# Performance work log

Hardware: AMD Instinct MI355X
Metric: run time of the kernel (lower is better)

## Reference

```python
import jax, jax.numpy as jnp
import numpy as np

BN_EPS = 1e-5


def setup_inputs() -> dict:
    key = jax.random.key(0)
    ks = jax.random.split(key, 8)
    B, C, H, W = 8, 512, 48, 48
    P = 64
    s_in = 1.0 / np.sqrt(C)
    s_p = 1.0 / np.sqrt(P)
    return {
        "x": jax.random.normal(ks[0], (B, C, H, W), dtype=jnp.float32),
        "Wq": jax.random.uniform(ks[1], (P, C), jnp.float32, -s_in, s_in),
        "Wk": jax.random.uniform(ks[2], (P, C), jnp.float32, -s_in, s_in),
        "Wv": jax.random.uniform(ks[3], (C, C), jnp.float32, -s_in, s_in),
        "align_w": jax.random.uniform(ks[4], (P,), jnp.float32, -s_p, s_p),
        "Wfc": jax.random.uniform(ks[5], (C, C), jnp.float32, -s_in, s_in),
        "bfc": jax.random.uniform(ks[6], (C,), jnp.float32, -s_in, s_in),
        "gamma": jnp.ones((C,), jnp.float32),
        "beta": jnp.zeros((C,), jnp.float32),
    }


def reference(x, Wq, Wk, Wv, align_w, Wfc, bfc, gamma, beta):
    B, C, H, W = x.shape
    N = H * W
    px = jnp.transpose(x.reshape(B, C, N), (0, 2, 1))  # [B, N, C]

    q = jnp.tanh(px @ Wq.T)  # [B, N, P]
    k = jnp.tanh(px @ Wk.T)  # [B, N, P]
    v = px @ Wv.T            # [B, N, C]

    # align(q_i * k_j) = sum_p q[b,i,p] * k[b,j,p] * align_w[p]
    scores = jnp.einsum('bip,bjp,p->bij', q, k, align_w)  # [B, N, N]
    attn = jax.nn.softmax(scores, axis=2)

    content = px + attn @ v           # [B, N, C]
    content = content @ Wfc.T + bfc   # fc
    c = jnp.transpose(content, (0, 2, 1)).reshape(B, C, H, W)

    # BatchNorm2d in training mode: batch statistics over (B, H, W), biased var
    mean = jnp.mean(c, axis=(0, 2, 3), keepdims=True)
    var = jnp.var(c, axis=(0, 2, 3), keepdims=True)
    g = gamma.reshape(1, C, 1, 1)
    b = beta.reshape(1, C, 1, 1)
    out = g * (c - mean) * jax.lax.rsqrt(var + BN_EPS) + b
    return jax.nn.relu(out)
```

## Files before the change

kernel.cpp:

```cpp
#include <hip/hip_runtime.h>
#include <stdint.h>

#define BB 8
#define CC 512
#define NN 2304
#define NT16 (NN / 16)
#define NT32 (NN / 32)
#define CT32 (CC / 32)
#define NYB 48

typedef float f32x4 __attribute__((ext_vector_type(4)));
typedef short s16x8 __attribute__((ext_vector_type(8)));

__device__ __forceinline__ unsigned short f2bf(float f) {
  union { float f; uint32_t u; } v; v.f = f;
  uint32_t u = v.u;
  return (unsigned short)((u + 0x7FFFu + ((u >> 16) & 1u)) >> 16);
}
__device__ __forceinline__ float bf2f(unsigned short b) {
  union { uint32_t u; float f; } v; v.u = ((uint32_t)b) << 16;
  return v.f;
}


__global__ void k_prep_w(const float* __restrict__ Wq, const float* __restrict__ Wk,
                         const float* __restrict__ Wv, const float* __restrict__ Wfc,
                         unsigned short* __restrict__ wcat_t, unsigned short* __restrict__ wfc_t) {
  int idx = blockIdx.x * 256 + threadIdx.x;
  const int tot_cat = 640 * 512;
  if (idx < tot_cat) {
    int tile = idx >> 9, inner = idx & 511;
    int j = (tile >> 4) * 16 + (inner >> 5);
    int k = (tile & 15) * 32 + (inner & 31);
    float v = (j < 64) ? Wq[j * 512 + k] : ((j < 128) ? Wk[(j - 64) * 512 + k] : Wv[(j - 128) * 512 + k]);
    wcat_t[idx] = f2bf(v);
  } else if (idx < tot_cat + 512 * 512) {
    int i2 = idx - tot_cat;
    int tile = i2 >> 9, inner = i2 & 511;
    int j = (tile >> 4) * 16 + (inner >> 5);
    int k = (tile & 15) * 32 + (inner & 31);
    wfc_t[i2] = f2bf(Wfc[j * 512 + k]);
  }
}

__global__ void k_px(const float* __restrict__ x, unsigned short* __restrict__ px_t) {
  __shared__ float t[32][33];
  int b = blockIdx.x;
  int nb = blockIdx.y * 32;
  int cb = blockIdx.z * 32;
  int lane = threadIdx.x & 31;
  int row = threadIdx.x >> 5;
  const float* xb = x + (size_t)b * CC * NN;
  for (int rr = 0; rr < 4; rr++) {
    int c = cb + row + 8 * rr;
    t[row + 8 * rr][lane] = xb[(size_t)c * NN + nb + lane];
  }
  __syncthreads();
  int rbase = (b * NN + nb) >> 4;
  int ct = cb >> 5;
  for (int rr = 0; rr < 4; rr++) {
    int nl = row + 8 * rr;
    size_t off = ((size_t)(rbase + (nl >> 4)) * CT32 + ct) * 512 + (nl & 15) * 32 + lane;
    px_t[off] = f2bf(t[lane][nl]);
  }
}

__global__ __launch_bounds__(256, 2) void k_qkv(const unsigned short* __restrict__ px_t,
                                                const unsigned short* __restrict__ wcat_t,
                                                const float* __restrict__ align_w,
                                                unsigned short* __restrict__ q_t,
                                                unsigned short* __restrict__ k_t,
                                                unsigned short* __restrict__ v_row) {
  int b = blockIdx.x;
  int nb = blockIdx.y * 64;
  int jb0 = blockIdx.z * 128;
  int tid = threadIdx.x;
  int w = tid >> 6, l = tid & 63, l15 = l & 15, lq = l >> 4;
  int jw = jb0 + 32 * w;
  int loff = l15 * 32 + 8 * lq;
  int rA = (b * NN + nb) >> 4;
  f32x4 acc[4][2];
  for (int mf = 0; mf < 4; mf++) for (int nf = 0; nf < 2; nf++) acc[mf][nf] = (f32x4){0.f, 0.f, 0.f, 0.f};
  for (int kk = 0; kk < 16; kk++) {
    s16x8 a[4], bbf[2];
    for (int mf = 0; mf < 4; mf++)
      a[mf] = *(const s16x8*)(px_t + ((size_t)(rA + mf) * CT32 + kk) * 512 + loff);
    for (int nf = 0; nf < 2; nf++)
      bbf[nf] = *(const s16x8*)(wcat_t + ((size_t)((jw >> 4) + nf) * CT32 + kk) * 512 + loff);
    for (int mf = 0; mf < 4; mf++)
      for (int nf = 0; nf < 2; nf++)
        acc[mf][nf] = __builtin_amdgcn_mfma_f32_16x16x32_bf16(a[mf], bbf[nf], acc[mf][nf], 0, 0, 0);
  }
  for (int mf = 0; mf < 4; mf++)
    for (int nf = 0; nf < 2; nf++)
      for (int r = 0; r < 4; r++) {
        int j = jw + 16 * nf + l15;
        int nl = 4 * lq + r;
        float v = acc[mf][nf][r];
        if (j < 128) { v = tanhf(v); if (j < 64) v *= align_w[j]; }
        unsigned short bv = f2bf(v);
        if (j < 64)
          q_t[((size_t)(rA + mf) * 2 + (j >> 5)) * 512 + nl * 32 + (j & 31)] = bv;
        else if (j < 128) {
          int jj = j - 64;
          k_t[((size_t)(rA + mf) * 2 + (jj >> 5)) * 512 + nl * 32 + (jj & 31)] = bv;
        } else {
          v_row[((size_t)(b * NN) + nb + 16 * mf + nl) * 512 + (j - 128)] = bv;
        }
      }
}

__global__ void k_vt(const unsigned short* __restrict__ v_row, unsigned short* __restrict__ vt_t) {
  __shared__ uint32_t t[32][33];
  int b = blockIdx.x;
  int nb = blockIdx.y * 32;
  int cb = blockIdx.z * 32;
  int lane = threadIdx.x & 31;
  int row = threadIdx.x >> 5;
  const unsigned short* src = v_row + (size_t)b * NN * 512;
  for (int rr = 0; rr < 4; rr++) {
    int n = nb + row + 8 * rr;
    t[row + 8 * rr][lane] = (uint32_t)src[(size_t)n * 512 + cb + lane];
  }
  __syncthreads();
  unsigned short* dst = vt_t + (size_t)b * (CC / 16) * NT32 * 512;
  for (int rr = 0; rr < 4; rr++) {
    int c = cb + row + 8 * rr;
    size_t off = ((size_t)(c >> 4) * NT32 + (nb >> 5)) * 512 + (c & 15) * 32 + lane;
    dst[off] = (unsigned short)t[lane][row + 8 * rr];
  }
}

__global__ __launch_bounds__(256, 3) void k_attn(const unsigned short* __restrict__ q_t,
                                                 const unsigned short* __restrict__ k_t,
                                                 const unsigned short* __restrict__ vt_t,
                                                 unsigned short* __restrict__ px_t ) {
  __shared__ __align__(16) unsigned short e_s[2][48 * 64];
  __shared__ float rs_s[4][48];
  int b = blockIdx.x;
  int ib = blockIdx.y * 48;
  int ch = blockIdx.z * 256;
  int tid = threadIdx.x;
  int w = tid >> 6, l = tid & 63, l15 = l & 15, lq = l >> 4;
  int c0 = ch + 64 * w;
  int loff = l15 * 32 + 8 * lq;
  int rQ = (b * NN + ib) >> 4;
  int ktb = b * NT16;
  const unsigned short* vb = vt_t + (size_t)b * (CC / 16) * NT32 * 512;

  s16x8 qa[3][2];
  for (int mf = 0; mf < 3; mf++)
    for (int ks = 0; ks < 2; ks++)
      qa[mf][ks] = *(const s16x8*)(q_t + ((size_t)(rQ + mf) * 2 + ks) * 512 + loff);

  f32x4 acc[3][4];
  for (int mf = 0; mf < 3; mf++) for (int nf = 0; nf < 4; nf++) acc[mf][nf] = (f32x4){0.f, 0.f, 0.f, 0.f};
  float rs[3][4];
  for (int mf = 0; mf < 3; mf++) for (int r = 0; r < 4; r++) rs[mf][r] = 0.f;

  s16x8 kf[2];
  for (int ks = 0; ks < 2; ks++)
    kf[ks] = *(const s16x8*)(k_t + ((size_t)(ktb + w) * 2 + ks) * 512 + loff);

  for (int jt = 0; jt < NN / 64; jt++) {
    int jtn = (jt < NN / 64 - 1) ? jt + 1 : jt;
    s16x8 vf[2][4];
    for (int ks = 0; ks < 2; ks++)
      for (int nf = 0; nf < 4; nf++)
        vf[ks][nf] = *(const s16x8*)(vb + ((size_t)((c0 >> 4) + nf) * NT32 + jt * 2 + ks) * 512 + loff);
    s16x8 kn[2];
    for (int ks = 0; ks < 2; ks++)
      kn[ks] = *(const s16x8*)(k_t + ((size_t)(ktb + jtn * 4 + w) * 2 + ks) * 512 + loff);
    f32x4 sc[3];
    for (int mf = 0; mf < 3; mf++) sc[mf] = (f32x4){0.f, 0.f, 0.f, 0.f};
    for (int ks = 0; ks < 2; ks++)
      for (int mf = 0; mf < 3; mf++)
        sc[mf] = __builtin_amdgcn_mfma_f32_16x16x32_bf16(qa[mf][ks], kf[ks], sc[mf], 0, 0, 0);
    char* ebuf = (char*)e_s[jt & 1];
    for (int mf = 0; mf < 3; mf++)
      for (int r = 0; r < 4; r++) {
        float e = __expf(sc[mf][r]);
        rs[mf][r] += e;
        int i = 16 * mf + 4 * lq + r;
        int byte = (i * 128 + (16 * w + l15) * 2) ^ ((i & 7) << 4);
        *(unsigned short*)(ebuf + byte) = f2bf(e);
      }
    asm volatile("s_waitcnt lgkmcnt(0)" ::: "memory");
    __builtin_amdgcn_s_barrier();
    __builtin_amdgcn_sched_barrier(0);
    for (int ks = 0; ks < 2; ks++) {
      s16x8 ef[3];
      for (int mf = 0; mf < 3; mf++) {
        int i = 16 * mf + l15;
        int byte = (i * 128 + 64 * ks + 16 * lq) ^ ((i & 7) << 4);
        ef[mf] = *(const s16x8*)(ebuf + byte);
      }
      for (int nf = 0; nf < 4; nf++)
        for (int mf = 0; mf < 3; mf++)
          acc[mf][nf] = __builtin_amdgcn_mfma_f32_16x16x32_bf16(ef[mf], vf[ks][nf], acc[mf][nf], 0, 0, 0);
    }
    kf[0] = kn[0];
    kf[1] = kn[1];
  }

  for (int mf = 0; mf < 3; mf++)
    for (int r = 0; r < 4; r++) {
      float v = rs[mf][r];
      v += __shfl_xor(v, 1); v += __shfl_xor(v, 2);
      v += __shfl_xor(v, 4); v += __shfl_xor(v, 8);
      rs[mf][r] = v;
    }
  if (l15 == 0)
    for (int mf = 0; mf < 3; mf++)
      for (int r = 0; r < 4; r++)
        rs_s[w][16 * mf + 4 * lq + r] = rs[mf][r];
  __syncthreads();
  float inv[3][4];
  for (int mf = 0; mf < 3; mf++)
    for (int r = 0; r < 4; r++) {
      int i = 16 * mf + 4 * lq + r;
      inv[mf][r] = 1.0f / (rs_s[0][i] + rs_s[1][i] + rs_s[2][i] + rs_s[3][i]);
    }
  for (int mf = 0; mf < 3; mf++)
    for (int nf = 0; nf < 4; nf++)
      for (int r = 0; r < 4; r++) {
        int i = 16 * mf + 4 * lq + r;
        int bn = b * NN + ib + i;
        int c = c0 + 16 * nf + l15;
        size_t off = ((size_t)(bn >> 4) * CT32 + (c >> 5)) * 512 + (bn & 15) * 32 + (c & 31);
        px_t[off] = f2bf(bf2f(px_t[off]) + acc[mf][nf][r] * inv[mf][r]);
      }
}

__global__ __launch_bounds__(256, 3) void k_fc(const unsigned short* __restrict__ px_t,
                                               const unsigned short* __restrict__ wfc_t,
                                               const float* __restrict__ bfc,
                                               float* __restrict__ out,
                                               float2* __restrict__ partials) {
  __shared__ float pss[4][32], psq[4][32];
  int cb = blockIdx.x * 32;
  int yb = blockIdx.y;
  int fb = yb * 384;
  int tid = threadIdx.x;
  int w = tid >> 6, l = tid & 63, l15 = l & 15, lq = l >> 4;
  int fw = fb + 96 * w;
  int loff = l15 * 32 + 8 * lq;
  f32x4 acc[2][6];
  for (int mf = 0; mf < 2; mf++) for (int nf = 0; nf < 6; nf++) acc[mf][nf] = (f32x4){0.f, 0.f, 0.f, 0.f};
  for (int kk = 0; kk < 16; kk++) {
    s16x8 a[2], bbf[6];
    for (int mf = 0; mf < 2; mf++)
      a[mf] = *(const s16x8*)(wfc_t + ((size_t)((cb >> 4) + mf) * CT32 + kk) * 512 + loff);
    for (int nf = 0; nf < 6; nf++)
      bbf[nf] = *(const s16x8*)(px_t + ((size_t)((fw >> 4) + nf) * CT32 + kk) * 512 + loff);
    for (int mf = 0; mf < 2; mf++)
      for (int nf = 0; nf < 6; nf++)
        acc[mf][nf] = __builtin_amdgcn_mfma_f32_16x16x32_bf16(a[mf], bbf[nf], acc[mf][nf], 0, 0, 0);
  }
  float s8[2][4], q8[2][4];
  for (int mf = 0; mf < 2; mf++)
    for (int r = 0; r < 4; r++) {
      int c2 = cb + 16 * mf + 4 * lq + r;
      float bias = bfc[c2];
      float s = 0.f, q = 0.f;
      for (int nf = 0; nf < 6; nf++) {
        float v = acc[mf][nf][r] + bias;
        int flat = fw + 16 * nf + l15;
        int b2 = flat / NN;
        int n = flat - b2 * NN;
        out[((size_t)b2 * CC + c2) * NN + n] = v;
        s += v; q += v * v;
      }
      s8[mf][r] = s; q8[mf][r] = q;
    }
  for (int mf = 0; mf < 2; mf++)
    for (int r = 0; r < 4; r++) {
      float s = s8[mf][r], q = q8[mf][r];
      s += __shfl_xor(s, 1); q += __shfl_xor(q, 1);
      s += __shfl_xor(s, 2); q += __shfl_xor(q, 2);
      s += __shfl_xor(s, 4); q += __shfl_xor(q, 4);
      s += __shfl_xor(s, 8); q += __shfl_xor(q, 8);
      s8[mf][r] = s; q8[mf][r] = q;
    }
  if (l15 == 0)
    for (int mf = 0; mf < 2; mf++)
      for (int r = 0; r < 4; r++) {
        int idx = 16 * mf + 4 * lq + r;
        pss[w][idx] = s8[mf][r];
        psq[w][idx] = q8[mf][r];
      }
  __syncthreads();
  if (tid < 32) {
    float s = pss[0][tid] + pss[1][tid] + pss[2][tid] + pss[3][tid];
    float q = psq[0][tid] + psq[1][tid] + psq[2][tid] + psq[3][tid];
    partials[(size_t)(cb + tid) * NYB + yb] = make_float2(s, q);
  }
}

__global__ void k_stats2(const float2* __restrict__ partials, const float* __restrict__ gamma,
                         const float* __restrict__ beta, float2* __restrict__ ab) {
  int c = blockIdx.x * 256 + threadIdx.x;
  if (c >= CC) return;
  float s = 0.f, q = 0.f;
  for (int i = 0; i < NYB; i++) {
    float2 p = partials[(size_t)c * NYB + i];
    s += p.x; q += p.y;
  }
  const float invn = 1.0f / (BB * NN);
  float mean = s * invn;
  float var = q * invn - mean * mean;
  float a = gamma[c] * rsqrtf(var + 1e-5f);
  ab[c] = make_float2(a, beta[c] - mean * a);
}

__global__ void k_bn(float* __restrict__ out, const float2* __restrict__ ab) {
  int idx = blockIdx.x * 256 + threadIdx.x;
  const int total = BB * CC * NN / 4;
  if (idx >= total) return;
  int c = (idx / (NN / 4)) & (CC - 1);
  float2 p = ab[c];
  f32x4 v = ((f32x4*)out)[idx];
  for (int i = 0; i < 4; i++) v[i] = fmaxf(0.f, v[i] * p.x + p.y);
  ((f32x4*)out)[idx] = v;
}

extern "C" void kernel_launch(void* const* d_in, const int* in_sizes, int n_in,
                              void* d_out, int out_size, void* d_ws, size_t ws_size,
                              hipStream_t stream) {
  const float* x = (const float*)d_in[0];
  const float* Wq = (const float*)d_in[1];
  const float* Wk = (const float*)d_in[2];
  const float* Wv = (const float*)d_in[3];
  const float* align_w = (const float*)d_in[4];
  const float* Wfc = (const float*)d_in[5];
  const float* bfc = (const float*)d_in[6];
  const float* gamma = (const float*)d_in[7];
  const float* beta = (const float*)d_in[8];
  float* out = (float*)d_out;

  char* ws = (char*)d_ws;
  const size_t sz_px = (size_t)BB * NN * CC * 2;
  const size_t sz_q = (size_t)BB * NN * 64 * 2;
  const size_t sz_vr = (size_t)BB * NN * CC * 2;
  unsigned short* px_t = (unsigned short*)(ws);
  unsigned short* q_t = (unsigned short*)(ws + sz_px);
  unsigned short* k_t = (unsigned short*)(ws + sz_px + sz_q);
  unsigned short* v_row = (unsigned short*)(ws + sz_px + 2 * sz_q);
  unsigned short* vt_t = (unsigned short*)(ws + sz_px + 2 * sz_q + sz_vr);
  unsigned short* wcat_t = (unsigned short*)(ws + sz_px + 2 * sz_q + 2 * sz_vr);
  unsigned short* wfc_t = (unsigned short*)(ws + sz_px + 2 * sz_q + 2 * sz_vr + 640 * 512 * 2);
  float2* partials = (float2*)(ws + sz_px + 2 * sz_q + 2 * sz_vr + 640 * 512 * 2 + 512 * 512 * 2);
  float2* ab = (float2*)((char*)partials + (size_t)CC * NYB * sizeof(float2));

  k_prep_w<<<(640 * 512 + 512 * 512 + 255) / 256, 256, 0, stream>>>(Wq, Wk, Wv, Wfc, wcat_t, wfc_t);
  k_px<<<dim3(BB, NN / 32, CC / 32), 256, 0, stream>>>(x, px_t);
  k_qkv<<<dim3(BB, NN / 64, 5), 256, 0, stream>>>(px_t, wcat_t, align_w, q_t, k_t, v_row);
  k_vt<<<dim3(BB, NN / 32, CC / 32), 256, 0, stream>>>(v_row, vt_t);
  k_attn<<<dim3(BB, NN / 48, 2), 256, 0, stream>>>(q_t, k_t, vt_t, px_t);
  k_fc<<<dim3(CC / 32, NYB), 256, 0, stream>>>(px_t, wfc_t, bfc, out, partials);
  k_stats2<<<2, 256, 0, stream>>>(partials, gamma, beta, ab);
  k_bn<<<(BB * CC * NN / 4 + 255) / 256, 256, 0, stream>>>(out, ab);
}
```

Baseline: 204.2 us.

## Software-pipeline attention loop: overlap score/exp of tile jt with PV of jt-1

Restructures the attention main loop into a prologue, steady state and epilogue. Each iteration now computes scores and exp for tile jt into one LDS buffer while doing the P·V MFMAs for tile jt-1 from the other buffer, carrying V fragments one iteration ahead in registers. The aim is to hide the LDS write→barrier→read latency and let exp/VALU work overlap with MFMA. The cost is more live registers (two sets of V fragments), which may lower occupancy.

```diff
diff --git a/kernel.cpp b/kernel.cpp
--- a/kernel.cpp
+++ b/kernel.cpp
@@ -162,21 +162,20 @@
   for (int ks = 0; ks < 2; ks++)
     kf[ks] = *(const s16x8*)(k_t + ((size_t)(ktb + w) * 2 + ks) * 512 + loff);
 
-  for (int jt = 0; jt < NN / 64; jt++) {
-    int jtn = (jt < NN / 64 - 1) ? jt + 1 : jt;
-    s16x8 vf[2][4];
-    for (int ks = 0; ks < 2; ks++)
-      for (int nf = 0; nf < 4; nf++)
-        vf[ks][nf] = *(const s16x8*)(vb + ((size_t)((c0 >> 4) + nf) * NT32 + jt * 2 + ks) * 512 + loff);
+  s16x8 vfp[2][4];
+  for (int ks = 0; ks < 2; ks++)
+    for (int nf = 0; nf < 4; nf++)
+      vfp[ks][nf] = *(const s16x8*)(vb + ((size_t)((c0 >> 4) + nf) * NT32 + 0 * 2 + ks) * 512 + loff);
+  {
     s16x8 kn[2];
     for (int ks = 0; ks < 2; ks++)
-      kn[ks] = *(const s16x8*)(k_t + ((size_t)(ktb + jtn * 4 + w) * 2 + ks) * 512 + loff);
+      kn[ks] = *(const s16x8*)(k_t + ((size_t)(ktb + 1 * 4 + w) * 2 + ks) * 512 + loff);
     f32x4 sc[3];
     for (int mf = 0; mf < 3; mf++) sc[mf] = (f32x4){0.f, 0.f, 0.f, 0.f};
     for (int ks = 0; ks < 2; ks++)
       for (int mf = 0; mf < 3; mf++)
         sc[mf] = __builtin_amdgcn_mfma_f32_16x16x32_bf16(qa[mf][ks], kf[ks], sc[mf], 0, 0, 0);
-    char* ebuf = (char*)e_s[jt & 1];
+    char* ebuf = (char*)e_s[0];
     for (int mf = 0; mf < 3; mf++)
       for (int r = 0; r < 4; r++) {
         float e = __expf(sc[mf][r]);
@@ -188,19 +187,67 @@
     asm volatile("s_waitcnt lgkmcnt(0)" ::: "memory");
     __builtin_amdgcn_s_barrier();
     __builtin_amdgcn_sched_barrier(0);
+    kf[0] = kn[0];
+    kf[1] = kn[1];
+  }
+
+  for (int jt = 1; jt < NN / 64; jt++) {
+    int jtn = (jt < NN / 64 - 1) ? jt + 1 : jt;
+    s16x8 vfc[2][4];
+    for (int ks = 0; ks < 2; ks++)
+      for (int nf = 0; nf < 4; nf++)
+        vfc[ks][nf] = *(const s16x8*)(vb + ((size_t)((c0 >> 4) + nf) * NT32 + jt * 2 + ks) * 512 + loff);
+    s16x8 kn[2];
+    for (int ks = 0; ks < 2; ks++)
+      kn[ks] = *(const s16x8*)(k_t + ((size_t)(ktb + jtn * 4 + w) * 2 + ks) * 512 + loff);
+    f32x4 sc[3];
+    for (int mf = 0; mf < 3; mf++) sc[mf] = (f32x4){0.f, 0.f, 0.f, 0.f};
+    for (int ks = 0; ks < 2; ks++)
+      for (int mf = 0; mf < 3; mf++)
+        sc[mf] = __builtin_amdgcn_mfma_f32_16x16x32_bf16(qa[mf][ks], kf[ks], sc[mf], 0, 0, 0);
+    char* ebuf_w = (char*)e_s[jt & 1];
+    for (int mf = 0; mf < 3; mf++)
+      for (int r = 0; r < 4; r++) {
+        float e = __expf(sc[mf][r]);
+        rs[mf][r] += e;
+        int i = 16 * mf + 4 * lq + r;
+        int byte = (i * 128 + (16 * w + l15) * 2) ^ ((i & 7) << 4);
+        *(unsigned short*)(ebuf_w + byte) = f2bf(e);
+      }
+    char* ebuf_r = (char*)e_s[(jt - 1) & 1];
     for (int ks = 0; ks < 2; ks++) {
       s16x8 ef[3];
       for (int mf = 0; mf < 3; mf++) {
         int i = 16 * mf + l15;
         int byte = (i * 128 + 64 * ks + 16 * lq) ^ ((i & 7) << 4);
-        ef[mf] = *(const s16x8*)(ebuf + byte);
+        ef[mf] = *(const s16x8*)(ebuf_r + byte);
       }
       for (int nf = 0; nf < 4; nf++)
         for (int mf = 0; mf < 3; mf++)
-          acc[mf][nf] = __builtin_amdgcn_mfma_f32_16x16x32_bf16(ef[mf], vf[ks][nf], acc[mf][nf], 0, 0, 0);
-    }
-    kf[0] = kn[0];
-    kf[1] = kn[1];
+          acc[mf][nf] = __builtin_amdgcn_mfma_f32_16x16x32_bf16(ef[mf], vfp[ks][nf], acc[mf][nf], 0, 0, 0);
+    }
+    asm volatile("s_waitcnt lgkmcnt(0)" ::: "memory");
+    __builtin_amdgcn_s_barrier();
+    __builtin_amdgcn_sched_barrier(0);
+    for (int ks = 0; ks < 2; ks++) {
+      kf[ks] = kn[ks];
+      for (int nf = 0; nf < 4; nf++) vfp[ks][nf] = vfc[ks][nf];
+    }
+  }
+
+  {
+    char* ebuf_r = (char*)e_s[(NN / 64 - 1) & 1];
+    for (int ks = 0; ks < 2; ks++) {
+      s16x8 ef[3];
+      for (int mf = 0; mf < 3; mf++) {
+        int i = 16 * mf + l15;
+        int byte = (i * 128 + 64 * ks + 16 * lq) ^ ((i & 7) << 4);
+        ef[mf] = *(const s16x8*)(ebuf_r + byte);
+      }
+      for (int nf = 0; nf < 4; nf++)
+        for (int mf = 0; mf < 3; mf++)
+          acc[mf][nf] = __builtin_amdgcn_mfma_f32_16x16x32_bf16(ef[mf], vfp[ks][nf], acc[mf][nf], 0, 0, 0);
+    }
   }
 
   for (int mf = 0; mf < 3; mf++)
```

Result: faster. 198.4 us (-2.8%).

## Restructure attention loop: transposed score MFMA, packed bf16 stores, unroll, setprio

Applied to the files above, without the earlier changes.

The attention kernel now computes scores with swapped MFMA operands, so each lane holds four consecutive key columns for one query row. Those can be packed into bf16 pairs with v_cvt_pk_bf16_f32 and written to LDS as a single 8-byte store, and the row-sum reduction shrinks to two shuffles. The key loop is unrolled by two with ping-pong K register buffers instead of copying, MFMA sections are wrapped in s_setprio, and a flattened 1D grid is ordered batch-first then channel half. These changes aim to cut LDS store count, VALU conversion work and register moves, at the cost of more code and register pressure.

```diff
diff --git a/kernel.cpp b/kernel.cpp
--- a/kernel.cpp
+++ b/kernel.cpp
@@ -137,9 +137,10 @@
                                                  unsigned short* __restrict__ px_t ) {
   __shared__ __align__(16) unsigned short e_s[2][48 * 64];
   __shared__ float rs_s[4][48];
-  int b = blockIdx.x;
-  int ib = blockIdx.y * 48;
-  int ch = blockIdx.z * 256;
+  int bid = blockIdx.x;
+  int b = bid & 7;
+  int ch = ((bid >> 3) & 1) * 256;
+  int ib = (bid >> 4) * 48;
   int tid = threadIdx.x;
   int w = tid >> 6, l = tid & 63, l15 = l & 15, lq = l >> 4;
   int c0 = ch + 64 * w;
@@ -155,65 +156,71 @@
 
   f32x4 acc[3][4];
   for (int mf = 0; mf < 3; mf++) for (int nf = 0; nf < 4; nf++) acc[mf][nf] = (f32x4){0.f, 0.f, 0.f, 0.f};
-  float rs[3][4];
-  for (int mf = 0; mf < 3; mf++) for (int r = 0; r < 4; r++) rs[mf][r] = 0.f;
-
-  s16x8 kf[2];
+  float rs[3] = {0.f, 0.f, 0.f};
+
+  s16x8 kf0[2], kf1[2];
   for (int ks = 0; ks < 2; ks++)
-    kf[ks] = *(const s16x8*)(k_t + ((size_t)(ktb + w) * 2 + ks) * 512 + loff);
-
-  for (int jt = 0; jt < NN / 64; jt++) {
+    kf0[ks] = *(const s16x8*)(k_t + ((size_t)(ktb + w) * 2 + ks) * 512 + loff);
+
+  auto step = [&](int jt, char* ebuf, s16x8 (&kfu)[2], s16x8 (&kfl)[2]) {
     int jtn = (jt < NN / 64 - 1) ? jt + 1 : jt;
     s16x8 vf[2][4];
     for (int ks = 0; ks < 2; ks++)
       for (int nf = 0; nf < 4; nf++)
         vf[ks][nf] = *(const s16x8*)(vb + ((size_t)((c0 >> 4) + nf) * NT32 + jt * 2 + ks) * 512 + loff);
-    s16x8 kn[2];
     for (int ks = 0; ks < 2; ks++)
-      kn[ks] = *(const s16x8*)(k_t + ((size_t)(ktb + jtn * 4 + w) * 2 + ks) * 512 + loff);
+      kfl[ks] = *(const s16x8*)(k_t + ((size_t)(ktb + jtn * 4 + w) * 2 + ks) * 512 + loff);
     f32x4 sc[3];
     for (int mf = 0; mf < 3; mf++) sc[mf] = (f32x4){0.f, 0.f, 0.f, 0.f};
+    __builtin_amdgcn_s_setprio(1);
     for (int ks = 0; ks < 2; ks++)
       for (int mf = 0; mf < 3; mf++)
-        sc[mf] = __builtin_amdgcn_mfma_f32_16x16x32_bf16(qa[mf][ks], kf[ks], sc[mf], 0, 0, 0);
-    char* ebuf = (char*)e_s[jt & 1];
-    for (int mf = 0; mf < 3; mf++)
-      for (int r = 0; r < 4; r++) {
-        float e = __expf(sc[mf][r]);
-        rs[mf][r] += e;
-        int i = 16 * mf + 4 * lq + r;
-        int byte = (i * 128 + (16 * w + l15) * 2) ^ ((i & 7) << 4);
-        *(unsigned short*)(ebuf + byte) = f2bf(e);
-      }
+        sc[mf] = __builtin_amdgcn_mfma_f32_16x16x32_bf16(kfu[ks], qa[mf][ks], sc[mf], 0, 0, 0);
+    __builtin_amdgcn_s_setprio(0);
+    for (int mf = 0; mf < 3; mf++) {
+      float e0 = __expf(sc[mf][0]), e1 = __expf(sc[mf][1]);
+      float e2 = __expf(sc[mf][2]), e3 = __expf(sc[mf][3]);
+      rs[mf] += (e0 + e1) + (e2 + e3);
+      uint32_t p0, p1;
+      asm("v_cvt_pk_bf16_f32 %0, %1, %2" : "=v"(p0) : "v"(e0), "v"(e1));
+      asm("v_cvt_pk_bf16_f32 %0, %1, %2" : "=v"(p1) : "v"(e2), "v"(e3));
+      int i_ = 16 * mf + l15;
+      int byte = (i_ * 128 + (16 * w + 4 * lq) * 2) ^ ((i_ & 7) << 4);
+      uint2 pp; pp.x = p0; pp.y = p1;
+      *(uint2*)(ebuf + byte) = pp;
+    }
     asm volatile("s_waitcnt lgkmcnt(0)" ::: "memory");
     __builtin_amdgcn_s_barrier();
     __builtin_amdgcn_sched_barrier(0);
     for (int ks = 0; ks < 2; ks++) {
       s16x8 ef[3];
       for (int mf = 0; mf < 3; mf++) {
-        int i = 16 * mf + l15;
-        int byte = (i * 128 + 64 * ks + 16 * lq) ^ ((i & 7) << 4);
-        ef[mf] = *(const s16x8*)(ebuf + byte);
-      }
+        int i_ = 16 * mf + l15;
+        int byte = (i_ * 128 + 64 * ks + 16 * lq) ^ ((i_ & 7) << 4);
+        ef[mf] = *(const s16x8*)((const char*)ebuf + byte);
+      }
+      __builtin_amdgcn_s_setprio(1);
       for (int nf = 0; nf < 4; nf++)
         for (int mf = 0; mf < 3; mf++)
           acc[mf][nf] = __builtin_amdgcn_mfma_f32_16x16x32_bf16(ef[mf], vf[ks][nf], acc[mf][nf], 0, 0, 0);
-    }
-    kf[0] = kn[0];
-    kf[1] = kn[1];
-  }
-
-  for (int mf = 0; mf < 3; mf++)
-    for (int r = 0; r < 4; r++) {
-      float v = rs[mf][r];
-      v += __shfl_xor(v, 1); v += __shfl_xor(v, 2);
-      v += __shfl_xor(v, 4); v += __shfl_xor(v, 8);
-      rs[mf][r] = v;
-    }
-  if (l15 == 0)
+      __builtin_amdgcn_s_setprio(0);
+    }
+  };
+
+  for (int jt = 0; jt < NN / 64; jt += 2) {
+    step(jt, (char*)e_s[0], kf0, kf1);
+    step(jt + 1, (char*)e_s[1], kf1, kf0);
+  }
+
+  for (int mf = 0; mf < 3; mf++) {
+    float v = rs[mf];
+    v += __shfl_xor(v, 16);
+    v += __shfl_xor(v, 32);
+    rs[mf] = v;
+  }
+  if (lq == 0)
     for (int mf = 0; mf < 3; mf++)
-      for (int r = 0; r < 4; r++)
-        rs_s[w][16 * mf + 4 * lq + r] = rs[mf][r];
+      rs_s[w][16 * mf + l15] = rs[mf];
   __syncthreads();
   float inv[3][4];
   for (int mf = 0; mf < 3; mf++)
@@ -356,7 +363,7 @@
   k_px<<<dim3(BB, NN / 32, CC / 32), 256, 0, stream>>>(x, px_t);
   k_qkv<<<dim3(BB, NN / 64, 5), 256, 0, stream>>>(px_t, wcat_t, align_w, q_t, k_t, v_row);
   k_vt<<<dim3(BB, NN / 32, CC / 32), 256, 0, stream>>>(v_row, vt_t);
-  k_attn<<<dim3(BB, NN / 48, 2), 256, 0, stream>>>(q_t, k_t, vt_t, px_t);
+  k_attn<<<768, 256, 0, stream>>>(q_t, k_t, vt_t, px_t);
   k_fc<<<dim3(CC / 32, NYB), 256, 0, stream>>>(px_t, wfc_t, bfc, out, partials);
   k_stats2<<<2, 256, 0, stream>>>(partials, gamma, beta, ab);
   k_bn<<<(BB * CC * NN / 4 + 255) / 256, 256, 0, stream>>>(out, ab);
```

Measured after the change: 191.3 us. 1.07x faster.
